# Kernel optimization log

Measured on AMD Instinct MI355X. Metric: run time of the kernel, lower is better.

Reference implementation:

```python
import jax, jax.numpy as jnp
import numpy as np

N = 100000   # nodes
E = 1600000  # edges (before self-loops)
F_IN = 128
H = 128
C = 10       # classes
G = 256      # graphs in batch


def setup_inputs() -> dict:
    key = jax.random.key(0)
    ks = jax.random.split(key, 16)
    x = jax.random.normal(ks[0], (N, F_IN), dtype=jnp.float32)
    edge_index = jax.random.randint(ks[1], (2, E), 0, N, dtype=jnp.int32)
    batch = jnp.sort(jax.random.randint(ks[2], (N,), 0, G, dtype=jnp.int32))
    node_centrality = jax.random.uniform(ks[3], (N,), dtype=jnp.float32)
    edge_centrality = jax.random.uniform(ks[4], (E,), dtype=jnp.float32)
    s = 1.0 / np.sqrt(H)
    W1 = jax.random.normal(ks[5], (F_IN, H), dtype=jnp.float32) * s
    W2 = jax.random.normal(ks[6], (H, H), dtype=jnp.float32) * s
    W3 = jax.random.normal(ks[7], (H, H), dtype=jnp.float32) * s
    b1 = jnp.ones((H,), dtype=jnp.float32)  # bias init = torch.ones
    b2 = jnp.ones((H,), dtype=jnp.float32)
    b3 = jnp.ones((H,), dtype=jnp.float32)
    Wc = jax.random.normal(ks[8], (H, C), dtype=jnp.float32) * s
    bc = jnp.zeros((C,), dtype=jnp.float32)
    return {"x": x, "edge_index": edge_index, "batch": batch,
            "node_centrality": node_centrality, "edge_centrality": edge_centrality,
            "W1": W1, "b1": b1, "W2": W2, "b2": b2, "W3": W3, "b3": b3,
            "Wc": Wc, "bc": bc}


def reference(x, edge_index, batch, node_centrality, edge_centrality,
              W1, b1, W2, b2, W3, b3, Wc, bc):
    # add self-loops (edge_index is identical across layers)
    loops = jnp.arange(N, dtype=edge_index.dtype)
    row = jnp.concatenate([edge_index[0], loops])  # source (x_j gathered here)
    col = jnp.concatenate([edge_index[1], loops])  # target (aggregated here)
    # quantum norm: [edge_centrality; node_centrality] matches cat order in edge_update
    norm_quantum = jnp.concatenate([edge_centrality, node_centrality])
    # symmetric degree norm (degree of aggregation targets)
    deg = jax.ops.segment_sum(jnp.ones_like(col, dtype=x.dtype), col, num_segments=N)
    deg_inv_sqrt = jnp.where(deg > 0, deg ** -0.5, 0.0)
    norm = (deg_inv_sqrt[row] * deg_inv_sqrt[col] * norm_quantum)[:, None]  # [E+N, 1]

    for W, b in ((W1, b1), (W2, b2), (W3, b3)):
        h = x @ W                                   # [N, H]
        msg = norm * h[row]                         # gather + scale  [E+N, H]
        agg = jax.ops.segment_sum(msg, col, num_segments=N)  # scatter-add
        x = jax.nn.relu(agg + b)

    # global mean pool over graphs
    sums = jax.ops.segment_sum(x, batch, num_segments=G)            # [G, H]
    cnt = jax.ops.segment_sum(jnp.ones((N,), x.dtype), batch, num_segments=G)
    pooled = sums / jnp.maximum(cnt, 1.0)[:, None]
    return pooled @ Wc + bc  # [G, C]
```

## Files before the change

kernel.cpp:

```cpp
#include <hip/hip_runtime.h>
#include <hip/hip_bf16.h>

#define NN 100000
#define EE 1600000
#define HF 128
#define GG 256
#define CCLS 10

#define PSH 9
#define PTGT (1 << PSH)
#define NPART ((NN + PTGT - 1) >> PSH)
#define SLAB 9728
#define ACH 4096
#define PCH 32

typedef __attribute__((ext_vector_type(8))) short bf16x8;
typedef __attribute__((ext_vector_type(4))) float f32x4;

#define WT_PITCH 136

__device__ __forceinline__ float bflo(uint u) { return __uint_as_float(u << 16); }
__device__ __forceinline__ float bfhi(uint u) { return __uint_as_float(u & 0xffff0000u); }
__device__ __forceinline__ uint packbf(float a, float b) {
  __hip_bfloat16 x = __float2bfloat16(a), y = __float2bfloat16(b);
  return (uint)*(unsigned short*)&x | ((uint)*(unsigned short*)&y << 16);
}

__global__ __launch_bounds__(256) void k_zero(float* __restrict__ p, int n) {
  int i = blockIdx.x * 256 + threadIdx.x;
  if (i < n) p[i] = 0.f;
}

__global__ __launch_bounds__(256) void k_binA(const int* __restrict__ ei, const float* __restrict__ ec,
                                              int* __restrict__ part_tail, int2* __restrict__ stage) {
  __shared__ int cnt[NPART];
  __shared__ int base[NPART];
  const int tid = threadIdx.x;
  const int e0 = blockIdx.x * ACH;
  const int eend = min(e0 + ACH, EE);
  for (int t = tid; t < NPART; t += 256) cnt[t] = 0;
  __syncthreads();
  for (int e = e0 + tid; e < eend; e += 256) {
    int c = ei[EE + e];
    atomicAdd(&cnt[c >> PSH], 1);
  }
  __syncthreads();
  for (int t = tid; t < NPART; t += 256) {
    base[t] = (cnt[t] > 0) ? atomicAdd(&part_tail[t], cnt[t]) : 0;
  }
  __syncthreads();
  for (int t = tid; t < NPART; t += 256) cnt[t] = 0;
  __syncthreads();
  for (int e = e0 + tid; e < eend; e += 256) {
    int c = ei[EE + e];
    int r = ei[e];
    float w = ec[e];
    int p = c >> PSH, tl = c & (PTGT - 1);
    int rank = atomicAdd(&cnt[p], 1);
    stage[(size_t)p * SLAB + base[p] + rank] = make_int2(r | (tl << 17), __float_as_int(w));
  }
}

__global__ __launch_bounds__(256) void k_binCount(const int2* __restrict__ stage, const int* __restrict__ part_tail,
                                                  const float* __restrict__ nc, int* __restrict__ cnt,
                                                  float* __restrict__ dis, float* __restrict__ cself) {
  __shared__ int lcnt[PTGT];
  const int p = blockIdx.x;
  const int tid = threadIdx.x;
  const int t0 = p << PSH;
  const int tmax = min(PTGT, NN - t0);
  for (int t = tid; t < PTGT; t += 256) lcnt[t] = 0;
  __syncthreads();
  const int n = part_tail[p];
  const int2* sl = stage + (size_t)p * SLAB;
  for (int j = tid; j < n; j += 256) {
    atomicAdd(&lcnt[((uint)sl[j].x) >> 17], 1);
  }
  __syncthreads();
  for (int t = tid; t < tmax; t += 256) {
    int c = lcnt[t];
    cnt[t0 + t] = c;
    float d = (float)(c + 1);
    dis[t0 + t] = rsqrtf(d);
    cself[t0 + t] = nc[t0 + t] / d;
  }
}

__global__ __launch_bounds__(256) void k_scan1(const int* __restrict__ cnt, int* __restrict__ rowptr,
                                               int* __restrict__ bsum) {
  int tid = threadIdx.x;
  int i = blockIdx.x * 256 + tid;
  int val = (i < NN) ? cnt[i] : 0;
  int lane = tid & 63, w = tid >> 6;
  int v = val;
  #pragma unroll
  for (int off = 1; off < 64; off <<= 1) {
    int t = __shfl_up(v, off, 64);
    if (lane >= off) v += t;
  }
  __shared__ int wsum[4];
  if (lane == 63) wsum[w] = v;
  __syncthreads();
  int woff = 0;
  for (int j = 0; j < w; ++j) woff += wsum[j];
  if (i < NN) rowptr[i] = woff + v - val;
  if (tid == 255) bsum[blockIdx.x] = woff + v;
}

__global__ __launch_bounds__(512) void k_scan2(const int* __restrict__ bsum, int* __restrict__ bofs,
                                               int* __restrict__ rowptr, int nb) {
  __shared__ int s[512];
  int tid = threadIdx.x;
  int orig = (tid < nb) ? bsum[tid] : 0;
  s[tid] = orig;
  __syncthreads();
  for (int off = 1; off < 512; off <<= 1) {
    int t = (tid >= off) ? s[tid - off] : 0;
    __syncthreads();
    s[tid] += t;
    __syncthreads();
  }
  if (tid < nb) bofs[tid] = s[tid] - orig;
  if (tid == 511) rowptr[NN] = s[511];
}

__global__ __launch_bounds__(256) void k_scan3(int* __restrict__ rowptr, const int* __restrict__ bofs) {
  int i = blockIdx.x * 256 + threadIdx.x;
  if (i < NN) rowptr[i] += bofs[blockIdx.x];
}

__global__ __launch_bounds__(256) void k_binB(const int2* __restrict__ stage, const int* __restrict__ part_tail,
                                              const int* __restrict__ rowptr, const float* __restrict__ dis,
                                              int2* __restrict__ csr) {
  __shared__ int lcnt[PTGT];
  __shared__ float dsh[PTGT];
  const int p = blockIdx.x;
  const int tid = threadIdx.x;
  const int t0 = p << PSH;
  const int tmax = min(PTGT, NN - t0);
  for (int t = tid; t < tmax; t += 256) { lcnt[t] = 0; dsh[t] = dis[t0 + t]; }
  __syncthreads();
  const int n = part_tail[p];
  const int2* sl = stage + (size_t)p * SLAB;
  for (int j = tid; j < n; j += 256) {
    int2 en = sl[j];
    int tl = ((uint)en.x) >> 17;
    int r = en.x & 0x1FFFF;
    float coef = dis[r] * dsh[tl] * __int_as_float(en.y);
    int pos = rowptr[t0 + tl] + atomicAdd(&lcnt[tl], 1);
    csr[pos] = make_int2(r, __float_as_int(coef));
  }
}

template<int INF32>
__global__ __launch_bounds__(256) void k_gemm(const void* __restrict__ Xv, const float* __restrict__ W,
                                              uint* __restrict__ Hb) {
  __shared__ short Wt[128 * WT_PITCH];
  const int tid = threadIdx.x;
  #pragma unroll
  for (int t = 0; t < 32; ++t) {
    int idx = t * 256 + tid;
    int c = idx & 127, kp = idx >> 7;
    float w0 = W[(2 * kp) * 128 + c];
    float w1 = W[(2 * kp + 1) * 128 + c];
    *(uint*)&Wt[c * WT_PITCH + 2 * kp] = packbf(w0, w1);
  }
  __syncthreads();

  const int wv = tid >> 6, lane = tid & 63;
  const int r15 = lane & 15, kgrp = lane >> 4;
  const int n0 = blockIdx.x * 128 + wv * 16 + r15;
  const int n1 = n0 + 64;
  f32x4 acc[2][8] = {};

  #pragma unroll
  for (int kk = 0; kk < 4; ++kk) {
    const int kbase = kk * 32 + kgrp * 8;
    bf16x8 xf[2];
    #pragma unroll
    for (int t = 0; t < 2; ++t) {
      int n = t ? n1 : n0;
      if (n < NN) {
        if constexpr (INF32) {
          const float* xrow = (const float*)Xv + (size_t)n * 128 + kbase;
          float4 xa = *(const float4*)xrow;
          float4 xb = *(const float4*)(xrow + 4);
          uint4 pk;
          pk.x = packbf(xa.x, xa.y); pk.y = packbf(xa.z, xa.w);
          pk.z = packbf(xb.x, xb.y); pk.w = packbf(xb.z, xb.w);
          xf[t] = *(bf16x8*)&pk;
        } else {
          xf[t] = *(const bf16x8*)((const short*)Xv + (size_t)n * 128 + kbase);
        }
      } else {
        #pragma unroll
        for (int j = 0; j < 8; ++j) xf[t][j] = 0;
      }
    }
    #pragma unroll
    for (int cb = 0; cb < 8; ++cb) {
      bf16x8 wf = *(const bf16x8*)&Wt[(cb * 16 + r15) * WT_PITCH + kbase];
      acc[0][cb] = __builtin_amdgcn_mfma_f32_16x16x32_bf16(wf, xf[0], acc[0][cb], 0, 0, 0);
      acc[1][cb] = __builtin_amdgcn_mfma_f32_16x16x32_bf16(wf, xf[1], acc[1][cb], 0, 0, 0);
    }
  }

  #pragma unroll
  for (int t = 0; t < 2; ++t) {
    int n = t ? n1 : n0;
    if (n < NN) {
      #pragma unroll
      for (int cb = 0; cb < 8; ++cb) {
        uint2 o;
        o.x = packbf(acc[t][cb][0], acc[t][cb][1]);
        o.y = packbf(acc[t][cb][2], acc[t][cb][3]);
        *(uint2*)&Hb[(size_t)n * 64 + cb * 8 + kgrp * 2] = o;
      }
    }
  }
}

__global__ __launch_bounds__(64) void k_aggregate(const uint* __restrict__ Hu,
                                                  const int2* __restrict__ csr,
                                                  const int* __restrict__ rowptr,
                                                  const float* __restrict__ cself,
                                                  const float* __restrict__ bias,
                                                  uint* __restrict__ AGGB) {
  const int lane = threadIdx.x;
  const int i = blockIdx.x;
  float2 bb = *(const float2*)&bias[lane * 2];
  float acc0 = bb.x, acc1 = bb.y;
  float cs = cself[i];
  {
    uint u = Hu[(size_t)i * 64 + lane];
    acc0 += cs * bflo(u);
    acc1 += cs * bfhi(u);
  }
  int k = rowptr[i], ke = rowptr[i + 1];
  for (; k + 7 < ke; k += 8) {
    int2 e0 = csr[k],     e1 = csr[k + 1], e2 = csr[k + 2], e3 = csr[k + 3];
    int2 e4 = csr[k + 4], e5 = csr[k + 5], e6 = csr[k + 6], e7 = csr[k + 7];
    uint u0 = Hu[(size_t)e0.x * 64 + lane];
    uint u1 = Hu[(size_t)e1.x * 64 + lane];
    uint u2 = Hu[(size_t)e2.x * 64 + lane];
    uint u3 = Hu[(size_t)e3.x * 64 + lane];
    uint u4 = Hu[(size_t)e4.x * 64 + lane];
    uint u5 = Hu[(size_t)e5.x * 64 + lane];
    uint u6 = Hu[(size_t)e6.x * 64 + lane];
    uint u7 = Hu[(size_t)e7.x * 64 + lane];
    float c0 = __int_as_float(e0.y), c1 = __int_as_float(e1.y);
    float c2 = __int_as_float(e2.y), c3 = __int_as_float(e3.y);
    float c4 = __int_as_float(e4.y), c5 = __int_as_float(e5.y);
    float c6 = __int_as_float(e6.y), c7 = __int_as_float(e7.y);
    acc0 += c0 * bflo(u0); acc1 += c0 * bfhi(u0);
    acc0 += c1 * bflo(u1); acc1 += c1 * bfhi(u1);
    acc0 += c2 * bflo(u2); acc1 += c2 * bfhi(u2);
    acc0 += c3 * bflo(u3); acc1 += c3 * bfhi(u3);
    acc0 += c4 * bflo(u4); acc1 += c4 * bfhi(u4);
    acc0 += c5 * bflo(u5); acc1 += c5 * bfhi(u5);
    acc0 += c6 * bflo(u6); acc1 += c6 * bfhi(u6);
    acc0 += c7 * bflo(u7); acc1 += c7 * bfhi(u7);
  }
  for (; k < ke; ++k) {
    int2 e0 = csr[k];
    float c0 = __int_as_float(e0.y);
    uint u0 = Hu[(size_t)e0.x * 64 + lane];
    acc0 += c0 * bflo(u0); acc1 += c0 * bfhi(u0);
  }
  AGGB[(size_t)i * 64 + lane] = packbf(fmaxf(acc0, 0.f), fmaxf(acc1, 0.f));
}

__global__ __launch_bounds__(64) void k_pool(const uint* __restrict__ Hb, const int* __restrict__ batch,
                                             float* __restrict__ pool, float* __restrict__ cntg) {
  const int f = threadIdx.x;
  const int n0 = blockIdx.x * PCH;
  const int nh = min(PCH, NN - n0);
  int g = batch[n0];
  float a0 = 0.f, a1 = 0.f;
  int run = 0;
  for (int base = 0; base < nh; base += 8) {
    const int m = min(8, nh - base);
    uint u[8];
    #pragma unroll
    for (int j = 0; j < 8; ++j)
      if (j < m) u[j] = Hb[(size_t)(n0 + base + j) * 64 + f];
    #pragma unroll
    for (int j = 0; j < 8; ++j) {
      if (j < m) {
        int gn = batch[n0 + base + j];
        if (gn != g) {
          atomicAdd(&pool[(size_t)g * 128 + 2 * f], a0);
          atomicAdd(&pool[(size_t)g * 128 + 2 * f + 1], a1);
          if (f == 0) atomicAdd(&cntg[g], (float)run);
          a0 = a1 = 0.f; run = 0; g = gn;
        }
        a0 += bflo(u[j]); a1 += bfhi(u[j]);
        run++;
      }
    }
  }
  atomicAdd(&pool[(size_t)g * 128 + 2 * f], a0);
  atomicAdd(&pool[(size_t)g * 128 + 2 * f + 1], a1);
  if (f == 0) atomicAdd(&cntg[g], (float)run);
}

__global__ __launch_bounds__(64) void k_head(const float* __restrict__ pool, const float* __restrict__ cntg,
                                             const float* __restrict__ Wc, const float* __restrict__ bc,
                                             float* __restrict__ out) {
  int g = blockIdx.x;
  int lane = threadIdx.x;
  float inv = 1.f / fmaxf(cntg[g], 1.f);
  float p0 = pool[(size_t)g * 128 + lane] * inv;
  float p1 = pool[(size_t)g * 128 + 64 + lane] * inv;
  #pragma unroll
  for (int c = 0; c < CCLS; ++c) {
    float s = p0 * Wc[lane * CCLS + c] + p1 * Wc[(lane + 64) * CCLS + c];
    s += __shfl_down(s, 32, 64);
    s += __shfl_down(s, 16, 64);
    s += __shfl_down(s, 8, 64);
    s += __shfl_down(s, 4, 64);
    s += __shfl_down(s, 2, 64);
    s += __shfl_down(s, 1, 64);
    if (lane == 0) out[g * CCLS + c] = s + bc[c];
  }
}

extern "C" void kernel_launch(void* const* d_in, const int* in_sizes, int n_in,
                              void* d_out, int out_size, void* d_ws, size_t ws_size,
                              hipStream_t stream) {
  const float* x  = (const float*)d_in[0];
  const int* ei   = (const int*)d_in[1];
  const int* batch = (const int*)d_in[2];
  const float* nc = (const float*)d_in[3];
  const float* ec = (const float*)d_in[4];
  const float* W1 = (const float*)d_in[5];
  const float* b1 = (const float*)d_in[6];
  const float* W2 = (const float*)d_in[7];
  const float* b2 = (const float*)d_in[8];
  const float* W3 = (const float*)d_in[9];
  const float* b3 = (const float*)d_in[10];
  const float* Wc = (const float*)d_in[11];
  const float* bc = (const float*)d_in[12];
  float* out = (float*)d_out;

  char* ws = (char*)d_ws;
  const size_t BH = (size_t)NN * 64 * 4;
  uint* hbuf = (uint*)(ws);
  uint* aggb = (uint*)(ws + BH);
  int2* csr  = (int2*)(ws + 2 * BH);
  int2* stage = (int2*)(ws + 2 * BH + (size_t)EE * 8);
  char* p = ws + 2 * BH + (size_t)EE * 8 + (size_t)NPART * SLAB * 8;
  int*   deg_cnt  = (int*)(p);                p += (size_t)NN * 4;
  int*   part_tail= (int*)(p);                p += 1024;
  float* dis      = (float*)(p);              p += (size_t)NN * 4;
  float* cself    = (float*)(p);              p += (size_t)NN * 4;
  int*   rowptr   = (int*)(p);                p += ((size_t)NN + 32) * 4;
  int*   bsum     = (int*)(p);                p += 2048;
  int*   bofs     = (int*)(p);                p += 2048;
  float* pool     = (float*)(p);              p += (size_t)GG * 128 * 4;
  float* cntg     = (float*)(p);              p += (size_t)GG * 4;

  const int ZN2 = GG * 128 + GG;
  const int nb_scan = (NN + 255) / 256;
  const int nbinA = (EE + ACH - 1) / ACH;

  k_zero<<<1, 256, 0, stream>>>((float*)part_tail, 256);
  k_zero<<<(ZN2 + 255) / 256, 256, 0, stream>>>(pool, ZN2);
  k_binA<<<nbinA, 256, 0, stream>>>(ei, ec, part_tail, stage);
  k_binCount<<<NPART, 256, 0, stream>>>(stage, part_tail, nc, deg_cnt, dis, cself);
  k_scan1<<<nb_scan, 256, 0, stream>>>(deg_cnt, rowptr, bsum);
  k_scan2<<<1, 512, 0, stream>>>(bsum, bofs, rowptr, nb_scan);
  k_scan3<<<nb_scan, 256, 0, stream>>>(rowptr, bofs);
  k_binB<<<NPART, 256, 0, stream>>>(stage, part_tail, rowptr, dis, csr);

  const float* Ws[3] = {W1, W2, W3};
  const float* bs[3] = {b1, b2, b3};
  const int gemm_grid = (NN + 127) / 128;
  for (int l = 0; l < 3; ++l) {
    if (l == 0) k_gemm<1><<<gemm_grid, 256, 0, stream>>>((const void*)x, Ws[l], hbuf);
    else        k_gemm<0><<<gemm_grid, 256, 0, stream>>>((const void*)aggb, Ws[l], hbuf);
    k_aggregate<<<NN, 64, 0, stream>>>(hbuf, csr, rowptr, cself, bs[l], aggb);
  }

  k_pool<<<(NN + PCH - 1) / PCH, 64, 0, stream>>>(aggb, batch, pool, cntg);
  k_head<<<GG, 64, 0, stream>>>(pool, cntg, Wc, bc, out);
}
```

Before: 332.6 us.

## Split aggregation across two waves and fold row-pointer scan into binning

The aggregation kernel now runs 128 threads per node: two wavefronts each take half the edge list and combine partial sums through shared memory, with an extra 4-edge unrolled tail. This adds memory-level parallelism per node for the gather-bound loop, at the cost of a block barrier and LDS traffic. The three-kernel prefix scan over degrees is replaced by a partition-level scan plus an in-block scan inside the counting kernel. The two zeroing launches are merged into one.

```diff
diff --git a/kernel.cpp b/kernel.cpp
--- a/kernel.cpp
+++ b/kernel.cpp
@@ -26,9 +26,11 @@
   return (uint)*(unsigned short*)&x | ((uint)*(unsigned short*)&y << 16);
 }
 
-__global__ __launch_bounds__(256) void k_zero(float* __restrict__ p, int n) {
+__global__ __launch_bounds__(256) void k_zero2(int* __restrict__ a, int na, float* __restrict__ b, int nb) {
   int i = blockIdx.x * 256 + threadIdx.x;
-  if (i < n) p[i] = 0.f;
+  if (i < na) a[i] = 0;
+  i -= na;
+  if (i >= 0 && i < nb) b[i] = 0.f;
 }
 
 __global__ __launch_bounds__(256) void k_binA(const int* __restrict__ ei, const float* __restrict__ ec,
@@ -61,10 +63,29 @@
   }
 }
 
+__global__ __launch_bounds__(256) void k_scanP(const int* __restrict__ part_tail, int* __restrict__ pbase,
+                                               int* __restrict__ rowptr) {
+  __shared__ int s[256];
+  int tid = threadIdx.x;
+  int orig = (tid < NPART) ? part_tail[tid] : 0;
+  s[tid] = orig;
+  __syncthreads();
+  for (int off = 1; off < 256; off <<= 1) {
+    int t = (tid >= off) ? s[tid - off] : 0;
+    __syncthreads();
+    s[tid] += t;
+    __syncthreads();
+  }
+  if (tid < NPART) pbase[tid] = s[tid] - orig;
+  if (tid == 255) rowptr[NN] = s[255];
+}
+
 __global__ __launch_bounds__(256) void k_binCount(const int2* __restrict__ stage, const int* __restrict__ part_tail,
-                                                  const float* __restrict__ nc, int* __restrict__ cnt,
-                                                  float* __restrict__ dis, float* __restrict__ cself) {
+                                                  const int* __restrict__ pbase, const float* __restrict__ nc,
+                                                  float* __restrict__ dis, float* __restrict__ cself,
+                                                  int* __restrict__ rowptr) {
   __shared__ int lcnt[PTGT];
+  __shared__ int wsum[4];
   const int p = blockIdx.x;
   const int tid = threadIdx.x;
   const int t0 = p << PSH;
@@ -77,20 +98,8 @@
     atomicAdd(&lcnt[((uint)sl[j].x) >> 17], 1);
   }
   __syncthreads();
-  for (int t = tid; t < tmax; t += 256) {
-    int c = lcnt[t];
-    cnt[t0 + t] = c;
-    float d = (float)(c + 1);
-    dis[t0 + t] = rsqrtf(d);
-    cself[t0 + t] = nc[t0 + t] / d;
-  }
-}
-
-__global__ __launch_bounds__(256) void k_scan1(const int* __restrict__ cnt, int* __restrict__ rowptr,
-                                               int* __restrict__ bsum) {
-  int tid = threadIdx.x;
-  int i = blockIdx.x * 256 + tid;
-  int val = (i < NN) ? cnt[i] : 0;
+  int c0 = lcnt[2 * tid], c1 = lcnt[2 * tid + 1];
+  int val = c0 + c1;
   int lane = tid & 63, w = tid >> 6;
   int v = val;
   #pragma unroll
@@ -98,35 +107,24 @@
     int t = __shfl_up(v, off, 64);
     if (lane >= off) v += t;
   }
-  __shared__ int wsum[4];
   if (lane == 63) wsum[w] = v;
   __syncthreads();
   int woff = 0;
   for (int j = 0; j < w; ++j) woff += wsum[j];
-  if (i < NN) rowptr[i] = woff + v - val;
-  if (tid == 255) bsum[blockIdx.x] = woff + v;
-}
-
-__global__ __launch_bounds__(512) void k_scan2(const int* __restrict__ bsum, int* __restrict__ bofs,
-                                               int* __restrict__ rowptr, int nb) {
-  __shared__ int s[512];
-  int tid = threadIdx.x;
-  int orig = (tid < nb) ? bsum[tid] : 0;
-  s[tid] = orig;
-  __syncthreads();
-  for (int off = 1; off < 512; off <<= 1) {
-    int t = (tid >= off) ? s[tid - off] : 0;
-    __syncthreads();
-    s[tid] += t;
-    __syncthreads();
-  }
-  if (tid < nb) bofs[tid] = s[tid] - orig;
-  if (tid == 511) rowptr[NN] = s[511];
-}
-
-__global__ __launch_bounds__(256) void k_scan3(int* __restrict__ rowptr, const int* __restrict__ bofs) {
-  int i = blockIdx.x * 256 + threadIdx.x;
-  if (i < NN) rowptr[i] += bofs[blockIdx.x];
+  int ex = woff + v - val + pbase[p];
+  int t = 2 * tid;
+  if (t < tmax) {
+    rowptr[t0 + t] = ex;
+    float d = (float)(c0 + 1);
+    dis[t0 + t] = rsqrtf(d);
+    cself[t0 + t] = nc[t0 + t] / d;
+  }
+  if (t + 1 < tmax) {
+    rowptr[t0 + t + 1] = ex + c0;
+    float d = (float)(c1 + 1);
+    dis[t0 + t + 1] = rsqrtf(d);
+    cself[t0 + t + 1] = nc[t0 + t + 1] / d;
+  }
 }
 
 __global__ __launch_bounds__(256) void k_binB(const int2* __restrict__ stage, const int* __restrict__ part_tail,
@@ -220,24 +218,31 @@
   }
 }
 
-__global__ __launch_bounds__(64) void k_aggregate(const uint* __restrict__ Hu,
-                                                  const int2* __restrict__ csr,
-                                                  const int* __restrict__ rowptr,
-                                                  const float* __restrict__ cself,
-                                                  const float* __restrict__ bias,
-                                                  uint* __restrict__ AGGB) {
-  const int lane = threadIdx.x;
+__global__ __launch_bounds__(128) void k_aggregate(const uint* __restrict__ Hu,
+                                                   const int2* __restrict__ csr,
+                                                   const int* __restrict__ rowptr,
+                                                   const float* __restrict__ cself,
+                                                   const float* __restrict__ bias,
+                                                   uint* __restrict__ AGGB) {
+  __shared__ float sm[128];
+  const int lane = threadIdx.x & 63;
+  const int w = threadIdx.x >> 6;
   const int i = blockIdx.x;
-  float2 bb = *(const float2*)&bias[lane * 2];
-  float acc0 = bb.x, acc1 = bb.y;
-  float cs = cself[i];
-  {
+  float acc0, acc1;
+  if (w == 0) {
+    float2 bb = *(const float2*)&bias[lane * 2];
     uint u = Hu[(size_t)i * 64 + lane];
-    acc0 += cs * bflo(u);
-    acc1 += cs * bfhi(u);
-  }
-  int k = rowptr[i], ke = rowptr[i + 1];
-  for (; k + 7 < ke; k += 8) {
+    float cs = cself[i];
+    acc0 = bb.x + cs * bflo(u);
+    acc1 = bb.y + cs * bfhi(u);
+  } else {
+    acc0 = acc1 = 0.f;
+  }
+  const int k0 = rowptr[i], ke = rowptr[i + 1];
+  const int mid = k0 + ((ke - k0 + 1) >> 1);
+  int k = w ? mid : k0;
+  const int kend = w ? ke : mid;
+  for (; k + 7 < kend; k += 8) {
     int2 e0 = csr[k],     e1 = csr[k + 1], e2 = csr[k + 2], e3 = csr[k + 3];
     int2 e4 = csr[k + 4], e5 = csr[k + 5], e6 = csr[k + 6], e7 = csr[k + 7];
     uint u0 = Hu[(size_t)e0.x * 64 + lane];
@@ -261,13 +266,33 @@
     acc0 += c6 * bflo(u6); acc1 += c6 * bfhi(u6);
     acc0 += c7 * bflo(u7); acc1 += c7 * bfhi(u7);
   }
-  for (; k < ke; ++k) {
+  if (k + 3 < kend) {
+    int2 e0 = csr[k], e1 = csr[k + 1], e2 = csr[k + 2], e3 = csr[k + 3];
+    uint u0 = Hu[(size_t)e0.x * 64 + lane];
+    uint u1 = Hu[(size_t)e1.x * 64 + lane];
+    uint u2 = Hu[(size_t)e2.x * 64 + lane];
+    uint u3 = Hu[(size_t)e3.x * 64 + lane];
+    float c0 = __int_as_float(e0.y), c1 = __int_as_float(e1.y);
+    float c2 = __int_as_float(e2.y), c3 = __int_as_float(e3.y);
+    acc0 += c0 * bflo(u0); acc1 += c0 * bfhi(u0);
+    acc0 += c1 * bflo(u1); acc1 += c1 * bfhi(u1);
+    acc0 += c2 * bflo(u2); acc1 += c2 * bfhi(u2);
+    acc0 += c3 * bflo(u3); acc1 += c3 * bfhi(u3);
+    k += 4;
+  }
+  for (; k < kend; ++k) {
     int2 e0 = csr[k];
     float c0 = __int_as_float(e0.y);
     uint u0 = Hu[(size_t)e0.x * 64 + lane];
     acc0 += c0 * bflo(u0); acc1 += c0 * bfhi(u0);
   }
-  AGGB[(size_t)i * 64 + lane] = packbf(fmaxf(acc0, 0.f), fmaxf(acc1, 0.f));
+  if (w == 1) { sm[lane] = acc0; sm[64 + lane] = acc1; }
+  __syncthreads();
+  if (w == 0) {
+    acc0 += sm[lane];
+    acc1 += sm[64 + lane];
+    AGGB[(size_t)i * 64 + lane] = packbf(fmaxf(acc0, 0.f), fmaxf(acc1, 0.f));
+  }
 }
 
 __global__ __launch_bounds__(64) void k_pool(const uint* __restrict__ Hb, const int* __restrict__ batch,
@@ -350,27 +375,21 @@
   int2* csr  = (int2*)(ws + 2 * BH);
   int2* stage = (int2*)(ws + 2 * BH + (size_t)EE * 8);
   char* p = ws + 2 * BH + (size_t)EE * 8 + (size_t)NPART * SLAB * 8;
-  int*   deg_cnt  = (int*)(p);                p += (size_t)NN * 4;
   int*   part_tail= (int*)(p);                p += 1024;
+  int*   pbase    = (int*)(p);                p += 1024;
   float* dis      = (float*)(p);              p += (size_t)NN * 4;
   float* cself    = (float*)(p);              p += (size_t)NN * 4;
   int*   rowptr   = (int*)(p);                p += ((size_t)NN + 32) * 4;
-  int*   bsum     = (int*)(p);                p += 2048;
-  int*   bofs     = (int*)(p);                p += 2048;
   float* pool     = (float*)(p);              p += (size_t)GG * 128 * 4;
   float* cntg     = (float*)(p);              p += (size_t)GG * 4;
 
   const int ZN2 = GG * 128 + GG;
-  const int nb_scan = (NN + 255) / 256;
   const int nbinA = (EE + ACH - 1) / ACH;
 
-  k_zero<<<1, 256, 0, stream>>>((float*)part_tail, 256);
-  k_zero<<<(ZN2 + 255) / 256, 256, 0, stream>>>(pool, ZN2);
+  k_zero2<<<(256 + ZN2 + 255) / 256, 256, 0, stream>>>(part_tail, 256, pool, ZN2);
   k_binA<<<nbinA, 256, 0, stream>>>(ei, ec, part_tail, stage);
-  k_binCount<<<NPART, 256, 0, stream>>>(stage, part_tail, nc, deg_cnt, dis, cself);
-  k_scan1<<<nb_scan, 256, 0, stream>>>(deg_cnt, rowptr, bsum);
-  k_scan2<<<1, 512, 0, stream>>>(bsum, bofs, rowptr, nb_scan);
-  k_scan3<<<nb_scan, 256, 0, stream>>>(rowptr, bofs);
+  k_scanP<<<1, 256, 0, stream>>>(part_tail, pbase, rowptr);
+  k_binCount<<<NPART, 256, 0, stream>>>(stage, part_tail, pbase, nc, dis, cself, rowptr);
   k_binB<<<NPART, 256, 0, stream>>>(stage, part_tail, rowptr, dis, csr);
 
   const float* Ws[3] = {W1, W2, W3};
@@ -379,7 +398,7 @@
   for (int l = 0; l < 3; ++l) {
     if (l == 0) k_gemm<1><<<gemm_grid, 256, 0, stream>>>((const void*)x, Ws[l], hbuf);
     else        k_gemm<0><<<gemm_grid, 256, 0, stream>>>((const void*)aggb, Ws[l], hbuf);
-    k_aggregate<<<NN, 64, 0, stream>>>(hbuf, csr, rowptr, cself, bs[l], aggb);
+    k_aggregate<<<NN, 128, 0, stream>>>(hbuf, csr, rowptr, cself, bs[l], aggb);
   }
 
   k_pool<<<(NN + PCH - 1) / PCH, 64, 0, stream>>>(aggb, batch, pool, cntg);
```

New measurement: 400.8 us. 1.21x slower.
